# Performance work log

Measured on AMD Instinct MI355X. Metric: run time of the kernel, lower is better.

## Reference

```python
import jax, jax.numpy as jnp
import numpy as np

N_MODES = 64


def setup_inputs() -> dict:
    key = jax.random.key(0)
    k1, k2, k3 = jax.random.split(key, 3)
    B, Cin, S = 32, 128, 8192
    H, Hc, M = 4, 32, N_MODES  # n_heads, head_channels, n_modes (Cout = H*Hc = 128)
    x = jax.random.normal(k1, (B, Cin, S), dtype=jnp.float32)
    # per-head init scale: std = 0.01 * 2**h (matches _init_weights)
    scale = (0.01 * 2.0 ** jnp.arange(H, dtype=jnp.float32)).reshape(H, 1, 1, 1)
    w_real = jax.random.normal(k2, (H, Cin, Hc, M), dtype=jnp.float32) * scale
    w_imag = jax.random.normal(k3, (H, Cin, Hc, M), dtype=jnp.float32) * scale
    return {"x": x, "w_real": w_real, "w_imag": w_imag}


def reference(x, w_real, w_imag):
    B, Cin, S = x.shape
    H, _, Hc, M = w_real.shape
    Cout = H * Hc
    x_ft = jnp.fft.rfft(x, axis=-1)                 # [B, Cin, F] complex64
    F = x_ft.shape[-1]
    M = min(M, F)                                    # static
    w = (w_real + 1j * w_imag).astype(x_ft.dtype)    # [H, Cin, Hc, M]
    # fused batched complex contraction over all heads/modes at once
    out = jnp.einsum('bim,hiom->bhom', x_ft[:, :, :M], w[..., :M])  # [B, H, Hc, M]
    out = out.reshape(B, Cout, M)                    # head h -> channels [h*Hc, (h+1)*Hc)
    out_ft = jnp.zeros((B, Cout, F), dtype=x_ft.dtype).at[:, :, :M].set(out)
    return jnp.fft.irfft(out_ft, n=S, axis=-1)       # [B, Cout, S] float32
```

## Files before the change

### kernel.cpp

```cpp
#include <hip/hip_runtime.h>
#include <cstdio>

#define S_LEN 8192
#define NM 64

typedef short s8v __attribute__((ext_vector_type(8)));
typedef float f4  __attribute__((ext_vector_type(4)));
typedef _Float16 h8 __attribute__((ext_vector_type(8)));

static __device__ inline unsigned short f2bf(float f) {
    unsigned int u = __builtin_bit_cast(unsigned int, f);
    u = (u + 0x7FFFu + ((u >> 16) & 1u)) >> 16;
    return (unsigned short)u;
}
static __device__ inline float bf2f(unsigned short h) {
    unsigned int u = ((unsigned int)h) << 16;
    return __builtin_bit_cast(float, u);
}

#define SW32(r, k) (((r) * 32) + ((k) ^ ((((r) >> 1) & 3) << 3)))

static __device__ __forceinline__ void glds16(const void* g, void* l) {
    __builtin_amdgcn_global_load_lds(
        (const __attribute__((address_space(1))) unsigned int*)g,
        (__attribute__((address_space(3))) unsigned int*)l, 16, 0, 0);
}

__global__ __launch_bounds__(256) void gen_master(float* __restrict__ tab) {
    int p = blockIdx.x * 256 + threadIdx.x;
    tab[p] = cosf((float)p * (6.28318530717958647692f / (float)S_LEN));
}

__global__ __launch_bounds__(256) void gen_tables(const float* __restrict__ tab,
                                                  short* __restrict__ T1fH,
                                                  short* __restrict__ T1fL,
                                                  _Float16* __restrict__ Bimg) {
    int tid = blockIdx.x * 256 + threadIdx.x;
    {
        int tile = tid >> 12;
        int sb = tile >> 2, kc = tile & 3;
        int uw = tid & 4095;
        int c = uw >> 5, rest = uw & 31;
        int k = kc * 32 + rest;
        int s = sb * 128 + c;
        int m = k >> 1;
        int p = (m * s + ((k & 1) << 11)) & (S_LEN - 1);
        float v = tab[p];
        unsigned short h = f2bf(v);
        T1fH[tid] = (short)h;
        T1fL[tid] = (short)f2bf(v - bf2f(h));
    }
    {
        int tk = tid >> 13;
        int us = tid & 8191;
        int c = us >> 6;
        int wl = us & 63;
        int slot = wl >> 3, e = wl & 7;
        int k = ((slot ^ (c & 7)) << 3) | e;
        int kg = tk * 64 + k;
        int m = c >> 1;
        int p = (m * kg + ((c & 1) << 11)) & (S_LEN - 1);
        Bimg[tid] = (_Float16)tab[p];
    }
}

__global__ __launch_bounds__(512, 4) void dft_fwd_mfma(const float* __restrict__ x,
        const _Float16* __restrict__ Bimg, float* __restrict__ P) {
    __shared__ _Float16 abh[2][4096], abl[2][4096];
    __shared__ _Float16 bb[2][8192];
    const int t = threadIdx.x;
    const int lane = t & 63, w = t >> 6;
    const int rl = lane & 15, kq = lane >> 4;
    const int wr = w >> 2, wc = w & 3;
    const int row0 = blockIdx.x * 64;
    const int ks = blockIdx.y;
    const int rA = t >> 3, sA = t & 7;
    const size_t xrow = (size_t)(row0 + rA) * S_LEN + (size_t)ks * 1024 + (size_t)sA * 8;
    const int usA = rA * 64 + ((sA ^ (rA & 7)) << 3);
    const size_t bby = (size_t)ks * 16 * 16384 + (size_t)t * 32;

    f4 acc[2][2];
    #pragma unroll
    for (int i = 0; i < 2; ++i)
        #pragma unroll
        for (int j = 0; j < 2; ++j) acc[i][j] = (f4){0.f, 0.f, 0.f, 0.f};

    f4 aP[3][2];
    h8 bP[2][2];

    #define LA_(SC, A0, A1) { A0 = *(const f4*)&x[xrow + (size_t)(SC) * 64];       \
                              A1 = *(const f4*)&x[xrow + (size_t)(SC) * 64 + 4]; }
    #define LB_(SC, B0, B1) { const char* g = (const char*)Bimg + bby +            \
                                  (size_t)(SC) * 16384;                            \
                              B0 = *(const h8*)g; B1 = *(const h8*)(g + 16); }
    #define CV_(A0, A1, NXT) { h8 hv, lv;                                          \
        _Pragma("unroll")                                                          \
        for (int e = 0; e < 4; ++e) {                                              \
            float f = A0[e]; _Float16 hh = (_Float16)f;                            \
            hv[e] = hh; lv[e] = (_Float16)(f - (float)hh);                         \
        }                                                                          \
        _Pragma("unroll")                                                          \
        for (int e = 0; e < 4; ++e) {                                              \
            float f = A1[e]; _Float16 hh = (_Float16)f;                            \
            hv[4 + e] = hh; lv[4 + e] = (_Float16)(f - (float)hh);                 \
        }                                                                          \
        *(h8*)&abh[NXT][usA] = hv;                                                 \
        *(h8*)&abl[NXT][usA] = lv; }
    #define WB_(B0, B1, NXT) { *(h8*)&bb[NXT][t * 16] = B0;                        \
                               *(h8*)&bb[NXT][t * 16 + 8] = B1; }
    #define MM_(CUR) { _Pragma("unroll")                                           \
        for (int ksl = 0; ksl < 2; ++ksl) {                                        \
            const int sb_ = ksl * 4 + kq;                                          \
            h8 Ah0, Al0, Ah1, Al1, Bv0, Bv1;                                       \
            { int r = wr * 32 + rl;      int u = r * 64 + ((sb_ ^ (r & 7)) << 3);  \
              Ah0 = *(const h8*)&abh[CUR][u]; Al0 = *(const h8*)&abl[CUR][u]; }    \
            { int r = wr * 32 + 16 + rl; int u = r * 64 + ((sb_ ^ (r & 7)) << 3);  \
              Ah1 = *(const h8*)&abh[CUR][u]; Al1 = *(const h8*)&abl[CUR][u]; }    \
            { int c = wc * 32 + rl;      int u = c * 64 + ((sb_ ^ (c & 7)) << 3);  \
              Bv0 = *(const h8*)&bb[CUR][u]; }                                     \
            { int c = wc * 32 + 16 + rl; int u = c * 64 + ((sb_ ^ (c & 7)) << 3);  \
              Bv1 = *(const h8*)&bb[CUR][u]; }                                     \
            acc[0][0] = __builtin_amdgcn_mfma_f32_16x16x32_f16(Ah0, Bv0, acc[0][0], 0, 0, 0); \
            acc[0][1] = __builtin_amdgcn_mfma_f32_16x16x32_f16(Ah0, Bv1, acc[0][1], 0, 0, 0); \
            acc[1][0] = __builtin_amdgcn_mfma_f32_16x16x32_f16(Ah1, Bv0, acc[1][0], 0, 0, 0); \
            acc[1][1] = __builtin_amdgcn_mfma_f32_16x16x32_f16(Ah1, Bv1, acc[1][1], 0, 0, 0); \
            acc[0][0] = __builtin_amdgcn_mfma_f32_16x16x32_f16(Al0, Bv0, acc[0][0], 0, 0, 0); \
            acc[0][1] = __builtin_amdgcn_mfma_f32_16x16x32_f16(Al0, Bv1, acc[0][1], 0, 0, 0); \
            acc[1][0] = __builtin_amdgcn_mfma_f32_16x16x32_f16(Al1, Bv0, acc[1][0], 0, 0, 0); \
            acc[1][1] = __builtin_amdgcn_mfma_f32_16x16x32_f16(Al1, Bv1, acc[1][1], 0, 0, 0); \
        } }
    #define BAR_ __builtin_amdgcn_sched_barrier(0);                                \
        asm volatile("s_waitcnt lgkmcnt(0)" ::: "memory");                         \
        __builtin_amdgcn_sched_barrier(0);                                         \
        __builtin_amdgcn_s_barrier();                                              \
        __builtin_amdgcn_sched_barrier(0);

    {
        f4 t0a, t0b; h8 tb0a, tb0b;
        LA_(0, t0a, t0b) LB_(0, tb0a, tb0b)
        LA_(1, aP[1][0], aP[1][1]) LA_(2, aP[2][0], aP[2][1])
        LB_(1, bP[1][0], bP[1][1])
        __builtin_amdgcn_sched_barrier(0);
        CV_(t0a, t0b, 0) WB_(tb0a, tb0b, 0)
        BAR_
    }
    #pragma unroll
    for (int s = 0; s < 16; ++s) {
        if (s + 3 <= 15) LA_(s + 3, aP[(s + 3) % 3][0], aP[(s + 3) % 3][1])
        if (s + 2 <= 15) LB_(s + 2, bP[(s + 2) & 1][0], bP[(s + 2) & 1][1])
        __builtin_amdgcn_sched_barrier(0);
        if (s + 1 <= 15) { CV_(aP[(s + 1) % 3][0], aP[(s + 1) % 3][1], (s + 1) & 1)
                           WB_(bP[(s + 1) & 1][0], bP[(s + 1) & 1][1], (s + 1) & 1) }
        MM_(s & 1)
        if (s < 15) { BAR_ }
    }

    float* Pks = P + (size_t)ks * 524288;
    #pragma unroll
    for (int mf = 0; mf < 2; ++mf)
        #pragma unroll
        for (int nf = 0; nf < 2; ++nf)
            #pragma unroll
            for (int r = 0; r < 4; ++r)
                Pks[(size_t)(row0 + wr * 32 + mf * 16 + kq * 4 + r) * 128
                    + wc * 32 + nf * 16 + rl] = acc[mf][nf][r];
}

__global__ __launch_bounds__(256) void ksum_t(const float* __restrict__ P,
                                              float* __restrict__ Xt) {
    __shared__ float xt[32][130];
    const int row0 = blockIdx.x * 32;
    const int t = threadIdx.x;
    #pragma unroll
    for (int it = 0; it < 16; ++it) {
        int li = t + it * 256;
        int r = li >> 7, c = li & 127;
        float s = 0.f;
        #pragma unroll
        for (int ks = 0; ks < 8; ++ks)
            s += P[(size_t)ks * 524288 + (size_t)(row0 + r) * 128 + c];
        xt[r][c] = s;
    }
    __syncthreads();
    const int m = t >> 2, q = t & 3;
    #pragma unroll
    for (int j = 0; j < 8; ++j) {
        int r = q * 8 + j;
        float2 v = make_float2(xt[r][2 * m], xt[r][2 * m + 1]);
        *(float2*)&Xt[((size_t)m * 4096 + row0 + r) * 2] = v;
    }
}

__global__ __launch_bounds__(256) void wtrans(const float* __restrict__ w_real,
                                              const float* __restrict__ w_imag,
                                              float* __restrict__ wTr,
                                              float* __restrict__ wTi) {
    __shared__ float tile[64][65];
    const int io0 = blockIdx.x * 64;
    const int h = blockIdx.y >> 1;
    const float* src = (blockIdx.y & 1) ? w_imag : w_real;
    float* dst = (blockIdx.y & 1) ? wTi : wTr;
    const int t = threadIdx.x;
    #pragma unroll
    for (int it = 0; it < 16; ++it) {
        int li = t + it * 256;
        int r = li >> 6, c = li & 63;
        tile[r][c] = src[((size_t)h * 4096 + io0 + r) * 64 + c];
    }
    __syncthreads();
    #pragma unroll
    for (int it = 0; it < 16; ++it) {
        int li = t + it * 256;
        int mr = li >> 6, ioc = li & 63;
        dst[((size_t)h * 64 + mr) * 4096 + io0 + ioc] = tile[ioc][mr];
    }
}

__global__ __launch_bounds__(256) void mode_contract(const float* __restrict__ Xt,
        const float* __restrict__ wTr, const float* __restrict__ wTi,
        short* __restrict__ C2h, short* __restrict__ C2l) {
    __shared__ float xr[32][128], xi[32][128];
    __shared__ float wr[128][32], wi[128][32];
    const int m = blockIdx.x, h = blockIdx.y, t = threadIdx.x;
    #pragma unroll
    for (int it = 0; it < 16; ++it) {
        int li = t + it * 256;
        const float2 v = *(const float2*)&Xt[((size_t)m * 4096 + li) * 2];
        xr[li >> 7][li & 127] = v.x;
        xi[li >> 7][li & 127] = v.y;
        const size_t woff = (size_t)(h * 64 + m) * 4096 + li;
        wr[li >> 5][li & 31] = wTr[woff];
        wi[li >> 5][li & 31] = wTi[woff];
    }
    __syncthreads();
    const int o = t & 31;
    const int b0 = (t >> 5) * 4;
    float re[4] = {0.f, 0.f, 0.f, 0.f}, im[4] = {0.f, 0.f, 0.f, 0.f};
    for (int i = 0; i < 128; ++i) {
        float wrv = wr[i][o], wiv = wi[i][o];
        #pragma unroll
        for (int j = 0; j < 4; ++j) {
            float a = xr[b0 + j][i], c = xi[b0 + j][i];
            re[j] += a * wrv - c * wiv;
            im[j] += a * wiv + c * wrv;
        }
    }
    const float alpha = (m == 0) ? (1.0f / (float)S_LEN) : (2.0f / (float)S_LEN);
    const int kc = m >> 4;
    const int lk = (2 * m) & 31;
    #pragma unroll
    for (int j = 0; j < 4; ++j) {
        int row = (b0 + j) * 128 + h * 32 + o;
        float vr = alpha * re[j], vi = alpha * im[j];
        unsigned short hr = f2bf(vr), hi_ = f2bf(vi);
        float lr = vr - bf2f(hr), li_ = vi - bf2f(hi_);
        int rb = row >> 7, lr_ = row & 127;
        size_t ui = ((size_t)(rb * 4 + kc) * 4096 + SW32(lr_, lk)) >> 1;
        ((unsigned int*)C2h)[ui] = ((unsigned int)hi_ << 16) | hr;
        ((unsigned int*)C2l)[ui] = ((unsigned int)f2bf(li_) << 16) | f2bf(lr);
    }
}

__global__ __launch_bounds__(256, 2) void idft_mfma(const short* __restrict__ C2h,
        const short* __restrict__ C2l, const short* __restrict__ T1fH,
        const short* __restrict__ T1fL, float* __restrict__ y) {
    __shared__ short ah[4][4096], al[4][4096];
    const int t = threadIdx.x;
    const int lane = t & 63, w = t >> 6;
    const int rl = lane & 15, kq = lane >> 4;
    const int wm = (w >> 1) * 64, wn = (w & 1) * 64;
    const int sb = blockIdx.x, rb = blockIdx.y;

    #pragma unroll
    for (int kc = 0; kc < 4; ++kc) {
        const size_t ta = (size_t)(rb * 4 + kc) * 8192;
        const int wo = w * 2048 + lane * 16;
        glds16((const char*)C2h + ta + wo,        (char*)&ah[kc][0] + w * 2048);
        glds16((const char*)C2h + ta + wo + 1024, (char*)&ah[kc][0] + w * 2048 + 1024);
        glds16((const char*)C2l + ta + wo,        (char*)&al[kc][0] + w * 2048);
        glds16((const char*)C2l + ta + wo + 1024, (char*)&al[kc][0] + w * 2048 + 1024);
    }
    __syncthreads();

    f4 acc[4][4];
    #pragma unroll
    for (int i = 0; i < 4; ++i)
        #pragma unroll
        for (int j = 0; j < 4; ++j) acc[i][j] = (f4){0.f, 0.f, 0.f, 0.f};

    #pragma unroll
    for (int kc = 0; kc < 4; ++kc) {
        s8v Bh[4], Bl[4];
        const size_t tb = (size_t)(sb * 4 + kc) * 8192 + (size_t)rl * 64 + (size_t)kq * 16;
        #pragma unroll
        for (int nf = 0; nf < 4; ++nf) {
            const size_t off = tb + (size_t)(wn + nf * 16) * 64;
            Bh[nf] = *(const s8v*)((const char*)T1fH + off);
            Bl[nf] = *(const s8v*)((const char*)T1fL + off);
        }
        const int kk = kq * 8;
        s8v Ah[4], Al[4];
        #pragma unroll
        for (int mf = 0; mf < 4; ++mf) {
            int us = SW32(wm + mf * 16 + rl, kk);
            Ah[mf] = *(const s8v*)&ah[kc][us];
            Al[mf] = *(const s8v*)&al[kc][us];
        }
        #pragma unroll
        for (int mf = 0; mf < 4; ++mf)
            #pragma unroll
            for (int nf = 0; nf < 4; ++nf)
                acc[mf][nf] = __builtin_amdgcn_mfma_f32_16x16x32_bf16(Ah[mf], Bh[nf], acc[mf][nf], 0, 0, 0);
        #pragma unroll
        for (int mf = 0; mf < 4; ++mf)
            #pragma unroll
            for (int nf = 0; nf < 4; ++nf)
                acc[mf][nf] = __builtin_amdgcn_mfma_f32_16x16x32_bf16(Al[mf], Bh[nf], acc[mf][nf], 0, 0, 0);
        #pragma unroll
        for (int mf = 0; mf < 4; ++mf)
            #pragma unroll
            for (int nf = 0; nf < 4; ++nf)
                acc[mf][nf] = __builtin_amdgcn_mfma_f32_16x16x32_bf16(Ah[mf], Bl[nf], acc[mf][nf], 0, 0, 0);
    }

    #pragma unroll
    for (int mf = 0; mf < 4; ++mf) {
        int rr = rb * 128 + wm + mf * 16 + kq * 4;
        #pragma unroll
        for (int nf = 0; nf < 4; ++nf) {
            int c = sb * 128 + wn + nf * 16 + rl;
            #pragma unroll
            for (int r = 0; r < 4; ++r)
                __builtin_nontemporal_store(acc[mf][nf][r], &y[(size_t)(rr + r) * S_LEN + c]);
        }
    }
}

extern "C" void kernel_launch(void* const* d_in, const int* in_sizes, int n_in,
                              void* d_out, int out_size, void* d_ws, size_t ws_size,
                              hipStream_t stream) {
    const float* x      = (const float*)d_in[0];
    const float* w_real = (const float*)d_in[1];
    const float* w_imag = (const float*)d_in[2];
    float* y = (float*)d_out;

    const size_t TBL = (size_t)S_LEN * 128;
    char* w0 = (char*)d_ws;
    short* T1fH    = (short*)w0;
    short* T1fL    = T1fH + TBL;
    _Float16* Bimg = (_Float16*)(T1fL + TBL);
    float* Xt      = (float*)(Bimg + TBL);
    float* tab     = Xt + (size_t)64 * 4096 * 2;
    float* P       = tab + S_LEN;
    float* wTr     = P;
    float* wTi     = wTr + (size_t)4 * 64 * 4096;
    short* C2h     = (short*)(wTi + (size_t)4 * 64 * 4096);
    short* C2l     = C2h + TBL;
    const size_t TOTAL = (size_t)((char*)(P + 8 * (size_t)4096 * 128) - w0);
    if (ws_size < TOTAL) {
        fprintf(stderr, "kernel_launch: ws too small (%zu < %zu bytes)\n", ws_size, TOTAL);
        return;
    }

    gen_master<<<S_LEN / 256, 256, 0, stream>>>(tab);
    gen_tables<<<(S_LEN * 128) / 256, 256, 0, stream>>>(tab, T1fH, T1fL, Bimg);
    dft_fwd_mfma<<<dim3(64, 8), 512, 0, stream>>>(x, Bimg, P);
    ksum_t<<<128, 256, 0, stream>>>(P, Xt);
    wtrans<<<dim3(64, 8), 256, 0, stream>>>(w_real, w_imag, wTr, wTi);
    mode_contract<<<dim3(NM, 4), 256, 0, stream>>>(Xt, wTr, wTi, C2h, C2l);
    idft_mfma<<<dim3(64, 32), 256, 0, stream>>>(C2h, C2l, T1fH, T1fL, y);
}
```

Before: 117.0 us.

## Fuse split-K reduction into forward DFT via atomics and drop master cosine table

The forward DFT kernel now accumulates its split-K partial sums directly into the transposed Xt buffer with atomicAdd, replacing the P scratch buffer and the separate ksum_t reduce/transpose kernel; Xt is zeroed with a memset first. The gen_master kernel is removed and gen_tables computes cosf inline instead of reading a precomputed table. This cuts two kernel launches and the round trip of the partial-sum buffer through memory. In exchange it adds atomic contention across 8 K-splits, strided scattered atomic stores, a memset, and nondeterministic float summation order.

```diff
diff --git a/kernel.cpp b/kernel.cpp
--- a/kernel.cpp
+++ b/kernel.cpp
@@ -26,13 +26,7 @@
         (__attribute__((address_space(3))) unsigned int*)l, 16, 0, 0);
 }
 
-__global__ __launch_bounds__(256) void gen_master(float* __restrict__ tab) {
-    int p = blockIdx.x * 256 + threadIdx.x;
-    tab[p] = cosf((float)p * (6.28318530717958647692f / (float)S_LEN));
-}
-
-__global__ __launch_bounds__(256) void gen_tables(const float* __restrict__ tab,
-                                                  short* __restrict__ T1fH,
+__global__ __launch_bounds__(256) void gen_tables(short* __restrict__ T1fH,
                                                   short* __restrict__ T1fL,
                                                   _Float16* __restrict__ Bimg) {
     int tid = blockIdx.x * 256 + threadIdx.x;
@@ -45,7 +39,7 @@
         int s = sb * 128 + c;
         int m = k >> 1;
         int p = (m * s + ((k & 1) << 11)) & (S_LEN - 1);
-        float v = tab[p];
+        float v = cosf((float)p * (6.28318530717958647692f / (float)S_LEN));
         unsigned short h = f2bf(v);
         T1fH[tid] = (short)h;
         T1fL[tid] = (short)f2bf(v - bf2f(h));
@@ -60,12 +54,12 @@
         int kg = tk * 64 + k;
         int m = c >> 1;
         int p = (m * kg + ((c & 1) << 11)) & (S_LEN - 1);
-        Bimg[tid] = (_Float16)tab[p];
+        Bimg[tid] = (_Float16)cosf((float)p * (6.28318530717958647692f / (float)S_LEN));
     }
 }
 
 __global__ __launch_bounds__(512, 4) void dft_fwd_mfma(const float* __restrict__ x,
-        const _Float16* __restrict__ Bimg, float* __restrict__ P) {
+        const _Float16* __restrict__ Bimg, float* __restrict__ Xt) {
     __shared__ _Float16 abh[2][4096], abl[2][4096];
     __shared__ _Float16 bb[2][8192];
     const int t = threadIdx.x;
@@ -155,40 +149,18 @@
         if (s < 15) { BAR_ }
     }
 
-    float* Pks = P + (size_t)ks * 524288;
     #pragma unroll
     for (int mf = 0; mf < 2; ++mf)
         #pragma unroll
-        for (int nf = 0; nf < 2; ++nf)
-            #pragma unroll
-            for (int r = 0; r < 4; ++r)
-                Pks[(size_t)(row0 + wr * 32 + mf * 16 + kq * 4 + r) * 128
-                    + wc * 32 + nf * 16 + rl] = acc[mf][nf][r];
-}
-
-__global__ __launch_bounds__(256) void ksum_t(const float* __restrict__ P,
-                                              float* __restrict__ Xt) {
-    __shared__ float xt[32][130];
-    const int row0 = blockIdx.x * 32;
-    const int t = threadIdx.x;
-    #pragma unroll
-    for (int it = 0; it < 16; ++it) {
-        int li = t + it * 256;
-        int r = li >> 7, c = li & 127;
-        float s = 0.f;
-        #pragma unroll
-        for (int ks = 0; ks < 8; ++ks)
-            s += P[(size_t)ks * 524288 + (size_t)(row0 + r) * 128 + c];
-        xt[r][c] = s;
-    }
-    __syncthreads();
-    const int m = t >> 2, q = t & 3;
-    #pragma unroll
-    for (int j = 0; j < 8; ++j) {
-        int r = q * 8 + j;
-        float2 v = make_float2(xt[r][2 * m], xt[r][2 * m + 1]);
-        *(float2*)&Xt[((size_t)m * 4096 + row0 + r) * 2] = v;
-    }
+        for (int nf = 0; nf < 2; ++nf) {
+            const int c = wc * 32 + nf * 16 + rl;
+            float* dst = &Xt[((size_t)(c >> 1) * 4096) * 2 + (c & 1)];
+            #pragma unroll
+            for (int r = 0; r < 4; ++r) {
+                const int row = row0 + wr * 32 + mf * 16 + kq * 4 + r;
+                atomicAdd(dst + (size_t)row * 2, acc[mf][nf][r]);
+            }
+        }
 }
 
 __global__ __launch_bounds__(256) void wtrans(const float* __restrict__ w_real,
@@ -350,23 +322,20 @@
     short* T1fL    = T1fH + TBL;
     _Float16* Bimg = (_Float16*)(T1fL + TBL);
     float* Xt      = (float*)(Bimg + TBL);
-    float* tab     = Xt + (size_t)64 * 4096 * 2;
-    float* P       = tab + S_LEN;
-    float* wTr     = P;
+    float* wTr     = Xt + (size_t)64 * 4096 * 2;
     float* wTi     = wTr + (size_t)4 * 64 * 4096;
     short* C2h     = (short*)(wTi + (size_t)4 * 64 * 4096);
     short* C2l     = C2h + TBL;
-    const size_t TOTAL = (size_t)((char*)(P + 8 * (size_t)4096 * 128) - w0);
+    const size_t TOTAL = (size_t)((char*)(C2l + TBL) - w0);
     if (ws_size < TOTAL) {
         fprintf(stderr, "kernel_launch: ws too small (%zu < %zu bytes)\n", ws_size, TOTAL);
         return;
     }
 
-    gen_master<<<S_LEN / 256, 256, 0, stream>>>(tab);
-    gen_tables<<<(S_LEN * 128) / 256, 256, 0, stream>>>(tab, T1fH, T1fL, Bimg);
-    dft_fwd_mfma<<<dim3(64, 8), 512, 0, stream>>>(x, Bimg, P);
-    ksum_t<<<128, 256, 0, stream>>>(P, Xt);
+    hipMemsetAsync(Xt, 0, (size_t)64 * 4096 * 2 * sizeof(float), stream);
+    gen_tables<<<(S_LEN * 128) / 256, 256, 0, stream>>>(T1fH, T1fL, Bimg);
     wtrans<<<dim3(64, 8), 256, 0, stream>>>(w_real, w_imag, wTr, wTi);
+    dft_fwd_mfma<<<dim3(64, 8), 512, 0, stream>>>(x, Bimg, Xt);
     mode_contract<<<dim3(NM, 4), 256, 0, stream>>>(Xt, wTr, wTi, C2h, C2l);
     idft_mfma<<<dim3(64, 32), 256, 0, stream>>>(C2h, C2l, T1fH, T1fL, y);
 }
```

Result: slower. 149.0 us (+27.4%).
